# Optimization experiments

Measured on AMD Instinct MI355X. Metric: run time of the kernel, lower is better.

The kernel has to match this reference:

```python
import jax, jax.numpy as jnp
import numpy as np

N_NODES = 100000
N_EDGES = 600000
D = 128
L = 4
BN_EPS = 1e-5


def setup_inputs() -> dict:
    key = jax.random.key(0)
    ks = jax.random.split(key, 12)
    x = jax.random.normal(ks[0], (N_NODES, D), dtype=jnp.float32)
    edge_index = jax.random.randint(ks[1], (2, N_EDGES), 0, N_NODES, dtype=jnp.int64)
    edge_attr = jax.random.uniform(ks[2], (N_EDGES, 1), dtype=jnp.float32)
    s = 0.05
    return {
        'x': x,
        'edge_index': edge_index,
        'edge_attr': edge_attr,
        'We': jax.random.normal(ks[3], (L, 1, D), dtype=jnp.float32) * s,   # GINE edge projection Linear(1, D)
        'be': jnp.zeros((L, D), dtype=jnp.float32),
        'eps': jnp.zeros((L,), dtype=jnp.float32),                          # train_eps=True, init 0
        'W1': jax.random.normal(ks[4], (L, D, D), dtype=jnp.float32) * s,
        'b1': jnp.zeros((L, D), dtype=jnp.float32),
        'gamma': jnp.ones((L, D), dtype=jnp.float32),
        'beta': jnp.zeros((L, D), dtype=jnp.float32),
        'W2': jax.random.normal(ks[5], (L, D, D), dtype=jnp.float32) * s,
        'b2': jnp.zeros((L, D), dtype=jnp.float32),
    }


def _gine_layer(h, src, dst, edge_attr, We, be, eps, W1, b1, gamma, beta, W2, b2):
    n = h.shape[0]
    e = edge_attr @ We + be                       # [E, D] edge embedding
    m = jax.nn.relu(h[src] + e)                   # gather + add + relu (messages)
    agg = jax.ops.segment_sum(m, dst, num_segments=n)  # scatter-add to destination nodes
    z = (1.0 + eps) * h + agg
    # MLP: Linear -> BatchNorm1d (training stats) -> ReLU -> Linear
    z = z @ W1 + b1
    mu = jnp.mean(z, axis=0)
    var = jnp.var(z, axis=0)                      # biased var, as in torch BN training
    z = (z - mu) * jax.lax.rsqrt(var + BN_EPS) * gamma + beta
    z = jax.nn.relu(z)
    return z @ W2 + b2


def reference(x, edge_index, edge_attr, We, be, eps, W1, b1, gamma, beta, W2, b2):
    src, dst = edge_index[0], edge_index[1]
    h = x
    for l in range(L):
        z = _gine_layer(h, src, dst, edge_attr, We[l], be[l], eps[l],
                        W1[l], b1[l], gamma[l], beta[l], W2[l], b2[l])
        r = jax.nn.relu(z)
        h = r if l == 0 else h + r
    return h
```

## Files before the change

kernel.cpp:

```cpp
#include <hip/hip_runtime.h>

#define NN 100000
#define NE 600000
#define DD 128
#define NL 4
#define GB 512

typedef __attribute__((ext_vector_type(8))) short short8;
typedef __attribute__((ext_vector_type(4))) float float4v;
typedef __attribute__((ext_vector_type(2))) float f2;

__device__ inline unsigned short f2bf(float f) {
  union { float f; unsigned u; } v; v.f = f;
  unsigned r = v.u + 0x7fff + ((v.u >> 16) & 1);
  return (unsigned short)(r >> 16);
}
__device__ inline float bf2f(unsigned short u) {
  union { unsigned u; float f; } v; v.u = ((unsigned)u) << 16;
  return v.f;
}
__device__ inline f2 bfpair(unsigned u) {
  f2 r;
  r.x = __uint_as_float(u << 16);
  r.y = __uint_as_float(u & 0xffff0000u);
  return r;
}

__global__ void k_prep(const float* __restrict__ W1, const float* __restrict__ W2,
                       unsigned short* __restrict__ WT, int* __restrict__ counts,
                       float* __restrict__ stats4) {
  int i = blockIdx.x * 256 + threadIdx.x;
  if (i < NN) counts[i] = 0;
  if (i < NL * 256) stats4[i] = 0.f;
  if (i >= 8 * 16384) return;
  int m = i >> 14;
  int el = i & 16383;
  int k = el >> 7;
  int n = el & 127;
  const float* src = (m < 4) ? (W1 + (size_t)m * 16384) : (W2 + (size_t)(m - 4) * 16384);
  WT[(size_t)m * 16384 + n * 128 + k] = f2bf(src[k * 128 + n]);
}

__global__ void k_h2b(const float* __restrict__ src, unsigned short* __restrict__ dst,
                      const int* __restrict__ ei, int* __restrict__ counts) {
  int i = blockIdx.x * 256 + threadIdx.x;
  if (i < NE) atomicAdd(&counts[ei[NE + i]], 1);
  if (i >= NN * DD / 4) return;
  float4 v = ((const float4*)src)[i];
  ushort4 o;
  o.x = f2bf(v.x); o.y = f2bf(v.y); o.z = f2bf(v.z); o.w = f2bf(v.w);
  ((ushort4*)dst)[i] = o;
}

#define ST 256
#define SC 2
#define SB ((NN + ST * SC - 1) / (ST * SC))

__global__ void k_scan_part(const int* __restrict__ counts, int* __restrict__ row_ptr,
                            int* __restrict__ bsums) {
  __shared__ int s[ST];
  int b = blockIdx.x, t = threadIdx.x;
  int base = b * (ST * SC) + t * SC;
  int v0 = (base < NN) ? counts[base] : 0;
  int v1 = (base + 1 < NN) ? counts[base + 1] : 0;
  int tsum = v0 + v1;
  s[t] = tsum;
  __syncthreads();
  for (int d = 1; d < ST; d <<= 1) {
    int x = (t >= d) ? s[t - d] : 0;
    __syncthreads();
    s[t] += x;
    __syncthreads();
  }
  int excl = s[t] - tsum;
  if (base < NN) row_ptr[base] = excl;
  if (base + 1 < NN) row_ptr[base + 1] = excl + v0;
  if (t == ST - 1) bsums[b] = s[t];
}

__global__ void k_scan_bsum(const int* __restrict__ bsums, int* __restrict__ boffs,
                            int* __restrict__ row_ptr) {
  __shared__ int s[ST];
  int t = threadIdx.x;
  int v = (t < SB) ? bsums[t] : 0;
  s[t] = v;
  __syncthreads();
  for (int d = 1; d < ST; d <<= 1) {
    int x = (t >= d) ? s[t - d] : 0;
    __syncthreads();
    s[t] += x;
    __syncthreads();
  }
  if (t < SB) boffs[t] = s[t] - v;
  if (t == ST - 1) row_ptr[NN] = s[t];
}

__global__ void k_scan_add(const int* __restrict__ boffs, int* __restrict__ row_ptr,
                           int* __restrict__ off) {
  int b = blockIdx.x, t = threadIdx.x;
  int base = b * (ST * SC) + t * SC;
  int o = boffs[b];
  if (base < NN) { int v = row_ptr[base] + o; row_ptr[base] = v; off[base] = v; }
  if (base + 1 < NN) { int v = row_ptr[base + 1] + o; row_ptr[base + 1] = v; off[base + 1] = v; }
}

__global__ void k_fill(const int* __restrict__ ei, const float* __restrict__ attr,
                       int* __restrict__ off, int2* __restrict__ csr) {
  int e = blockIdx.x * 256 + threadIdx.x;
  if (e >= NE) return;
  int srcv = ei[e];
  int dstv = ei[NE + e];
  int idx = atomicAdd(&off[dstv], 1);
  csr[idx] = make_int2(srcv, __float_as_int(attr[e]));
}

#define CONS8(hv, at)                                                         \
  do {                                                                        \
    f2 av; av.x = (at); av.y = (at);                                          \
    f2 sx;                                                                    \
    sx = bfpair((hv).x) + (av * we01 + be01);                                 \
    a01 += __builtin_elementwise_max(sx, zero2);                              \
    sx = bfpair((hv).y) + (av * we23 + be23);                                 \
    a23 += __builtin_elementwise_max(sx, zero2);                              \
    sx = bfpair((hv).z) + (av * we45 + be45);                                 \
    a45 += __builtin_elementwise_max(sx, zero2);                              \
    sx = bfpair((hv).w) + (av * we67 + be67);                                 \
    a67 += __builtin_elementwise_max(sx, zero2);                              \
  } while (0)

#define LDROW(s) (*(const uint4*)(hb + (size_t)(s) * DD + d0))

__global__ __launch_bounds__(256) void k_agg(
    const unsigned short* __restrict__ hb,
    const int* __restrict__ row_ptr, const int2* __restrict__ csr,
    const float* __restrict__ We, const float* __restrict__ be,
    const float* __restrict__ epsp, unsigned short* __restrict__ zb) {
  const int tid0 = blockIdx.x * 256 + threadIdx.x;
  const int li = tid0 & 15;
  const int g0 = tid0 >> 4;
  const int NG = (gridDim.x * 256) >> 4;
  const int d0 = li * 8;

  const f2 we01 = *(const f2*)(We + d0);
  const f2 we23 = *(const f2*)(We + d0 + 2);
  const f2 we45 = *(const f2*)(We + d0 + 4);
  const f2 we67 = *(const f2*)(We + d0 + 6);
  const f2 be01 = *(const f2*)(be + d0);
  const f2 be23 = *(const f2*)(be + d0 + 2);
  const f2 be45 = *(const f2*)(be + d0 + 4);
  const f2 be67 = *(const f2*)(be + d0 + 6);
  const float ep = 1.f + epsp[0];
  f2 ep2; ep2.x = ep; ep2.y = ep;
  const f2 zero2 = {0.f, 0.f};

  for (int n = g0; n < NN; n += NG) {
    const int b = row_ptr[n], e = row_ptr[n + 1];
    const int deg = e - b;
    const int cnt = (deg < 16) ? deg : 16;
    int2 rec = (li < cnt) ? csr[b + li] : make_int2(0, 0);
    uint4 hs = LDROW(n);
    const int myidx = rec.x;
    const float myatt = __int_as_float(rec.y);
    f2 a01 = zero2, a23 = zero2, a45 = zero2, a67 = zero2;

    {
      int s0 = __shfl(myidx, 0, 16), s1 = __shfl(myidx, 1, 16);
      int s2 = __shfl(myidx, 2, 16), s3 = __shfl(myidx, 3, 16);
      int s4 = __shfl(myidx, 4, 16), s5 = __shfl(myidx, 5, 16);
      int s6 = __shfl(myidx, 6, 16), s7 = __shfl(myidx, 7, 16);
      float t0 = __shfl(myatt, 0, 16), t1 = __shfl(myatt, 1, 16);
      float t2 = __shfl(myatt, 2, 16), t3 = __shfl(myatt, 3, 16);
      float t4 = __shfl(myatt, 4, 16), t5 = __shfl(myatt, 5, 16);
      float t6 = __shfl(myatt, 6, 16), t7 = __shfl(myatt, 7, 16);
      uint4 h0 = LDROW(s0), h1 = LDROW(s1), h2 = LDROW(s2), h3 = LDROW(s3);
      uint4 h4 = LDROW(s4), h5 = LDROW(s5), h6 = LDROW(s6), h7 = LDROW(s7);
      if (cnt > 0) CONS8(h0, t0);
      if (cnt > 1) CONS8(h1, t1);
      if (cnt > 2) CONS8(h2, t2);
      if (cnt > 3) CONS8(h3, t3);
      if (cnt > 4) CONS8(h4, t4);
      if (cnt > 5) CONS8(h5, t5);
      if (cnt > 6) CONS8(h6, t6);
      if (cnt > 7) CONS8(h7, t7);
    }
    if (deg > 8) {
      int s0 = __shfl(myidx, 8, 16), s1 = __shfl(myidx, 9, 16);
      int s2 = __shfl(myidx, 10, 16), s3 = __shfl(myidx, 11, 16);
      int s4 = __shfl(myidx, 12, 16), s5 = __shfl(myidx, 13, 16);
      int s6 = __shfl(myidx, 14, 16), s7 = __shfl(myidx, 15, 16);
      float t0 = __shfl(myatt, 8, 16), t1 = __shfl(myatt, 9, 16);
      float t2 = __shfl(myatt, 10, 16), t3 = __shfl(myatt, 11, 16);
      float t4 = __shfl(myatt, 12, 16), t5 = __shfl(myatt, 13, 16);
      float t6 = __shfl(myatt, 14, 16), t7 = __shfl(myatt, 15, 16);
      uint4 h0 = LDROW(s0), h1 = LDROW(s1), h2 = LDROW(s2), h3 = LDROW(s3);
      uint4 h4 = LDROW(s4), h5 = LDROW(s5), h6 = LDROW(s6), h7 = LDROW(s7);
      if (cnt > 8)  CONS8(h0, t0);
      if (cnt > 9)  CONS8(h1, t1);
      if (cnt > 10) CONS8(h2, t2);
      if (cnt > 11) CONS8(h3, t3);
      if (cnt > 12) CONS8(h4, t4);
      if (cnt > 13) CONS8(h5, t5);
      if (cnt > 14) CONS8(h6, t6);
      if (cnt > 15) CONS8(h7, t7);
      for (int j = b + 16; j < e; j++) {
        int2 r2 = csr[j];
        float a = __int_as_float(r2.y);
        uint4 hv = LDROW(r2.x);
        CONS8(hv, a);
      }
    }

    f2 z01 = ep2 * bfpair(hs.x) + a01;
    f2 z23 = ep2 * bfpair(hs.y) + a23;
    f2 z45 = ep2 * bfpair(hs.z) + a45;
    f2 z67 = ep2 * bfpair(hs.w) + a67;
    uint4 o;
    o.x = (unsigned)f2bf(z01.x) | ((unsigned)f2bf(z01.y) << 16);
    o.y = (unsigned)f2bf(z23.x) | ((unsigned)f2bf(z23.y) << 16);
    o.z = (unsigned)f2bf(z45.x) | ((unsigned)f2bf(z45.y) << 16);
    o.w = (unsigned)f2bf(z67.x) | ((unsigned)f2bf(z67.y) << 16);
    *(uint4*)(zb + (size_t)n * DD + d0) = o;
  }
}

template <int MODE>
__global__ __launch_bounds__(512) void k_gemm(
    const unsigned short* __restrict__ Xb, const unsigned short* __restrict__ WT,
    const float* __restrict__ bias, float* __restrict__ stats,
    const float* __restrict__ gamma, const float* __restrict__ beta,
    const float* __restrict__ hprev, float* __restrict__ Yout,
    unsigned short* __restrict__ Ybf) {
  __shared__ unsigned short Wl[128 * 136];
  __shared__ unsigned short Xl[2][64 * 136];
  __shared__ float bns[256];
  const int tid = threadIdx.x;
  const int G = gridDim.x;
  const int NT = (NN + 63) >> 6;

  for (int i = tid; i < 2048; i += 512) {
    int rr = i >> 4, c = i & 15;
    *(uint4*)&Wl[rr * 136 + c * 8] = *(const uint4*)&WT[rr * 128 + c * 8];
  }

  const int lane = tid & 63;
  const int w = tid >> 6;
  const int m = lane & 15;
  const int quad = lane >> 4;
  const int rowblk = w & 3;
  const int ctbase = (w >> 2) * 4;

  float4 b4[4];
#pragma unroll
  for (int c = 0; c < 4; c++)
    b4[c] = *(const float4*)&bias[(ctbase + c) * 16 + quad * 4];

  const int c8 = tid & 15, rr16 = tid >> 4;
  float scl[8], sfl[8];
  if (MODE >= 1) {
    if (tid < 128) {
      const float invN = 1.f / (float)NN;
      float mu = stats[tid] * invN;
      float var = fmaxf(stats[128 + tid] * invN - mu * mu, 0.f);
      float xx = var + 1e-5f;
      float r = rsqrtf(xx);
      r = r * (1.5f - 0.5f * xx * r * r);
      float scale = gamma[tid] * r;
      bns[tid] = scale;
      bns[128 + tid] = beta[tid] - mu * scale;
    }
    __syncthreads();
#pragma unroll
    for (int j = 0; j < 8; j++) {
      scl[j] = bns[c8 * 8 + j];
      sfl[j] = bns[128 + c8 * 8 + j];
    }
  }

  uint4 xu[2];
  auto LOADR = [&](int t) {
    int r0 = t << 6;
#pragma unroll
    for (int it = 0; it < 2; it++) {
      int gr = r0 + rr16 + it * 32;
      xu[it] = (gr < NN) ? *(const uint4*)(Xb + (size_t)gr * DD + c8 * 8)
                         : make_uint4(0u, 0u, 0u, 0u);
    }
  };
  auto STORE_LDS = [&](int b) {
#pragma unroll
    for (int it = 0; it < 2; it++) {
      int row = rr16 + it * 32;
      uint4 u = xu[it];
      if (MODE >= 1) {
        unsigned p[4] = {u.x, u.y, u.z, u.w};
#pragma unroll
        for (int j = 0; j < 4; j++) {
          float lo = bf2f((unsigned short)(p[j] & 0xffffu));
          float hi = bf2f((unsigned short)(p[j] >> 16));
          lo = fmaxf(fmaf(lo, scl[2 * j], sfl[2 * j]), 0.f);
          hi = fmaxf(fmaf(hi, scl[2 * j + 1], sfl[2 * j + 1]), 0.f);
          p[j] = (unsigned)f2bf(lo) | ((unsigned)f2bf(hi) << 16);
        }
        u = make_uint4(p[0], p[1], p[2], p[3]);
      }
      *(uint4*)&Xl[b][row * 136 + c8 * 8] = u;
    }
  };

  float4v ssum[4], ssq[4];
  if (MODE == 0) {
#pragma unroll
    for (int c = 0; c < 4; c++) {
      ssum[c] = (float4v){0.f, 0.f, 0.f, 0.f};
      ssq[c] = (float4v){0.f, 0.f, 0.f, 0.f};
    }
  }

  const int t0 = blockIdx.x;
  LOADR(t0);
  STORE_LDS(0);
  if (t0 + G < NT) LOADR(t0 + G);
  __syncthreads();

  int buf = 0;
  for (int t = t0; t < NT; t += G) {
    const int nxt = t + G;
    if (nxt < NT) {
      STORE_LDS(buf ^ 1);
      if (nxt + G < NT) LOADR(nxt + G);
    }

    float4v acc[4];
#pragma unroll
    for (int c = 0; c < 4; c++)
      acc[c] = (float4v){b4[c].x, b4[c].y, b4[c].z, b4[c].w};

    const unsigned short* Ap = &Wl[(ctbase * 16 + m) * 136 + quad * 8];
    const unsigned short* Bp = &Xl[buf][(rowblk * 16 + m) * 136 + quad * 8];
#pragma unroll
    for (int q = 0; q < 4; q++) {
      short8 bfrag = *(const short8*)(Bp + q * 32);
#pragma unroll
      for (int c = 0; c < 4; c++) {
        short8 afrag = *(const short8*)(Ap + c * 16 * 136 + q * 32);
        acc[c] = __builtin_amdgcn_mfma_f32_16x16x32_bf16(afrag, bfrag, acc[c], 0, 0, 0);
      }
    }

    asm volatile("s_waitcnt lgkmcnt(0)" ::: "memory");
    __builtin_amdgcn_s_barrier();

    const int r = (t << 6) + rowblk * 16 + m;
    if (r < NN) {
      const size_t rb = (size_t)r * DD;
#pragma unroll
      for (int c = 0; c < 4; c++) {
        float4v v = acc[c];
        const int col = (ctbase + c) * 16 + quad * 4;
        if (MODE == 0) {
          ssum[c] += v;
          ssq[c] += v * v;
          ushort4 o;
          o.x = f2bf(v[0]); o.y = f2bf(v[1]); o.z = f2bf(v[2]); o.w = f2bf(v[3]);
          *(ushort4*)&Ybf[rb + col] = o;
        } else {
          v[0] = fmaxf(v[0], 0.f); v[1] = fmaxf(v[1], 0.f);
          v[2] = fmaxf(v[2], 0.f); v[3] = fmaxf(v[3], 0.f);
          if (MODE == 2) {
            float4 hp = *(const float4*)&hprev[rb + col];
            v[0] += hp.x; v[1] += hp.y; v[2] += hp.z; v[3] += hp.w;
          }
          *(float4v*)&Yout[rb + col] = v;
          if (Ybf) {
            ushort4 o;
            o.x = f2bf(v[0]); o.y = f2bf(v[1]); o.z = f2bf(v[2]); o.w = f2bf(v[3]);
            *(ushort4*)&Ybf[rb + col] = o;
          }
        }
      }
    }
    buf ^= 1;
  }

  if (MODE == 0) {
    float* sarr = (float*)Xl;
    float* sqarr = sarr + 512;
#pragma unroll
    for (int c = 0; c < 4; c++) {
      float4v s = ssum[c], s2 = ssq[c];
#pragma unroll
      for (int d = 1; d < 16; d <<= 1) {
#pragma unroll
        for (int j = 0; j < 4; j++) {
          s[j] += __shfl_xor(s[j], d);
          s2[j] += __shfl_xor(s2[j], d);
        }
      }
      if (m == 0) {
        *(float4v*)&sarr[w * 64 + c * 16 + quad * 4] = s;
        *(float4v*)&sqarr[w * 64 + c * 16 + quad * 4] = s2;
      }
    }
    __syncthreads();
    if (tid < 128) {
      const int ch = tid >> 6;
      const int cl = tid & 63;
      float s = 0.f, s2 = 0.f;
#pragma unroll
      for (int ww = 0; ww < 4; ww++) {
        s += sarr[(ch * 4 + ww) * 64 + cl];
        s2 += sqarr[(ch * 4 + ww) * 64 + cl];
      }
      atomicAdd(&stats[tid], s);
      atomicAdd(&stats[128 + tid], s2);
    }
  }
}

static inline size_t align256(size_t x) { return (x + 255) & ~(size_t)255; }

extern "C" void kernel_launch(void* const* d_in, const int* in_sizes, int n_in,
                              void* d_out, int out_size, void* d_ws, size_t ws_size,
                              hipStream_t stream) {
  const float* x     = (const float*)d_in[0];
  const int*   ei    = (const int*)d_in[1];
  const float* attr  = (const float*)d_in[2];
  const float* We    = (const float*)d_in[3];
  const float* be    = (const float*)d_in[4];
  const float* eps   = (const float*)d_in[5];
  const float* W1    = (const float*)d_in[6];
  const float* b1    = (const float*)d_in[7];
  const float* gamma = (const float*)d_in[8];
  const float* beta  = (const float*)d_in[9];
  const float* W2    = (const float*)d_in[10];
  const float* b2    = (const float*)d_in[11];
  float* out = (float*)d_out;

  char* w = (char*)d_ws;
  unsigned short* z2 = (unsigned short*)w; w += align256((size_t)NN * DD * 2);
  unsigned short* hb = (unsigned short*)w; w += align256((size_t)NN * DD * 2);
  unsigned short* zb = (unsigned short*)w; w += align256((size_t)NN * DD * 2);
  int*   row_ptr  = (int*)w;   w += align256((size_t)(NN + 1) * 4);
  int*   counts   = (int*)w;   w += align256((size_t)NN * 4);
  int*   off      = (int*)w;   w += align256((size_t)NN * 4);
  int2*  csr      = (int2*)w;  w += align256((size_t)NE * 8);
  float* stats4   = (float*)w; w += align256((size_t)NL * 256 * 4);
  int*   bsums    = (int*)w;   w += align256(ST * 4);
  int*   boffs    = (int*)w;   w += align256(ST * 4);
  unsigned short* WTb = (unsigned short*)w; w += align256((size_t)8 * 16384 * 2);

  k_prep<<<512, 256, 0, stream>>>(W1, W2, WTb, counts, stats4);
  k_h2b<<<(NN * DD / 4 + 255) / 256, 256, 0, stream>>>(x, hb, ei, counts);
  k_scan_part<<<SB, ST, 0, stream>>>(counts, row_ptr, bsums);
  k_scan_bsum<<<1, ST, 0, stream>>>(bsums, boffs, row_ptr);
  k_scan_add<<<SB, ST, 0, stream>>>(boffs, row_ptr, off);
  k_fill<<<(NE + 255) / 256, 256, 0, stream>>>(ei, attr, off, csr);

  for (int l = 0; l < NL; l++) {
    float* st = stats4 + (size_t)l * 256;
    k_agg<<<2048, 256, 0, stream>>>(
        hb, row_ptr, csr, We + l * DD, be + l * DD, eps + l, zb);
    k_gemm<0><<<GB, 512, 0, stream>>>(zb, WTb + (size_t)l * 16384, b1 + l * DD,
                                      st, nullptr, nullptr, nullptr, nullptr, z2);
    unsigned short* hbo = (l < NL - 1) ? hb : nullptr;
    if (l == 0)
      k_gemm<1><<<GB, 512, 0, stream>>>(z2, WTb + (size_t)(4 + l) * 16384, b2 + l * DD,
                                        st, gamma + l * DD, beta + l * DD,
                                        nullptr, out, hbo);
    else
      k_gemm<2><<<GB, 512, 0, stream>>>(z2, WTb + (size_t)(4 + l) * 16384, b2 + l * DD,
                                        st, gamma + l * DD, beta + l * DD,
                                        out, out, hbo);
  }
}
```

Before: 523.9 us.

## Build CSR via two-pass bucketed placement instead of global atomic fill

Replaces the per-edge global atomicAdd CSR fill with a two-phase scheme. Edges are first bucketed by destination block of 512 nodes using shared-memory atomics and coalesced writes to a staging buffer. A per-bucket kernel then places them into the final CSR using shared-memory cursors. This aims to cut scattered global atomics and random writes, at the cost of an extra pass over the edges and an extra NE*8-byte staging buffer.

```diff
diff --git a/kernel.cpp b/kernel.cpp
--- a/kernel.cpp
+++ b/kernel.cpp
@@ -5,6 +5,9 @@
 #define DD 128
 #define NL 4
 #define GB 512
+#define BKS 9
+#define NBK ((NN + 511) >> 9)
+#define CH 4096
 
 typedef __attribute__((ext_vector_type(8))) short short8;
 typedef __attribute__((ext_vector_type(4))) float float4v;
@@ -96,22 +99,83 @@
 }
 
 __global__ void k_scan_add(const int* __restrict__ boffs, int* __restrict__ row_ptr,
-                           int* __restrict__ off) {
+                           int* __restrict__ scur) {
   int b = blockIdx.x, t = threadIdx.x;
   int base = b * (ST * SC) + t * SC;
   int o = boffs[b];
-  if (base < NN) { int v = row_ptr[base] + o; row_ptr[base] = v; off[base] = v; }
-  if (base + 1 < NN) { int v = row_ptr[base + 1] + o; row_ptr[base + 1] = v; off[base + 1] = v; }
-}
-
-__global__ void k_fill(const int* __restrict__ ei, const float* __restrict__ attr,
-                       int* __restrict__ off, int2* __restrict__ csr) {
-  int e = blockIdx.x * 256 + threadIdx.x;
-  if (e >= NE) return;
-  int srcv = ei[e];
-  int dstv = ei[NE + e];
-  int idx = atomicAdd(&off[dstv], 1);
-  csr[idx] = make_int2(srcv, __float_as_int(attr[e]));
+  if (base < NN) {
+    int v = row_ptr[base] + o;
+    row_ptr[base] = v;
+    if ((base & 511) == 0) scur[base >> 9] = v;
+  }
+  if (base + 1 < NN) row_ptr[base + 1] += o;
+}
+
+__global__ __launch_bounds__(256) void k_bucket(
+    const int* __restrict__ ei, const float* __restrict__ attr,
+    int* __restrict__ scur, int2* __restrict__ staging) {
+  __shared__ int cnt[256], cnt2[256], base[256], gbase[256], s[256];
+  __shared__ int lpk[CH];
+  __shared__ int lat[CH];
+  __shared__ unsigned char lbk[CH];
+  const int t = threadIdx.x;
+  const int c0 = blockIdx.x * CH;
+  const int n = min(CH, NE - c0);
+  cnt[t] = 0;
+  cnt2[t] = 0;
+  __syncthreads();
+  for (int k = t; k < n; k += 256) {
+    int dst = ei[NE + c0 + k];
+    atomicAdd(&cnt[dst >> BKS], 1);
+  }
+  __syncthreads();
+  s[t] = cnt[t];
+  __syncthreads();
+  for (int d = 1; d < 256; d <<= 1) {
+    int x = (t >= d) ? s[t - d] : 0;
+    __syncthreads();
+    s[t] += x;
+    __syncthreads();
+  }
+  base[t] = s[t] - cnt[t];
+  if (cnt[t] > 0) gbase[t] = atomicAdd(&scur[t], cnt[t]);
+  __syncthreads();
+  for (int k = t; k < n; k += 256) {
+    int e = c0 + k;
+    int src = ei[e];
+    int dst = ei[NE + e];
+    int b = dst >> BKS;
+    int pos = base[b] + atomicAdd(&cnt2[b], 1);
+    lpk[pos] = src | ((dst & 511) << 17);
+    lat[pos] = __float_as_int(attr[e]);
+    lbk[pos] = (unsigned char)b;
+  }
+  __syncthreads();
+  for (int k = t; k < n; k += 256) {
+    int b = lbk[k];
+    staging[gbase[b] + (k - base[b])] = make_int2(lpk[k], lat[k]);
+  }
+}
+
+__global__ __launch_bounds__(256) void k_place(
+    const int* __restrict__ row_ptr, const int2* __restrict__ staging,
+    int2* __restrict__ csr) {
+  __shared__ int cur[512];
+  const int b = blockIdx.x;
+  const int n0 = b << BKS;
+  const int nb = min(512, NN - n0);
+  const int t = threadIdx.x;
+  for (int j = t; j < nb; j += 256) cur[j] = row_ptr[n0 + j];
+  __syncthreads();
+  const int s0 = row_ptr[n0];
+  const int s1 = row_ptr[n0 + nb];
+  for (int i = s0 + t; i < s1; i += 256) {
+    int2 r = staging[i];
+    int j = ((unsigned)r.x) >> 17;
+    int src = r.x & 0x1FFFF;
+    int slot = atomicAdd(&cur[j], 1);
+    csr[slot] = make_int2(src, r.y);
+  }
 }
 
 #define CONS8(hv, at)                                                         \
@@ -442,8 +506,9 @@
   unsigned short* zb = (unsigned short*)w; w += align256((size_t)NN * DD * 2);
   int*   row_ptr  = (int*)w;   w += align256((size_t)(NN + 1) * 4);
   int*   counts   = (int*)w;   w += align256((size_t)NN * 4);
-  int*   off      = (int*)w;   w += align256((size_t)NN * 4);
+  int*   scur     = (int*)w;   w += align256(256 * 4);
   int2*  csr      = (int2*)w;  w += align256((size_t)NE * 8);
+  int2*  staging  = (int2*)w;  w += align256((size_t)NE * 8);
   float* stats4   = (float*)w; w += align256((size_t)NL * 256 * 4);
   int*   bsums    = (int*)w;   w += align256(ST * 4);
   int*   boffs    = (int*)w;   w += align256(ST * 4);
@@ -453,8 +518,9 @@
   k_h2b<<<(NN * DD / 4 + 255) / 256, 256, 0, stream>>>(x, hb, ei, counts);
   k_scan_part<<<SB, ST, 0, stream>>>(counts, row_ptr, bsums);
   k_scan_bsum<<<1, ST, 0, stream>>>(bsums, boffs, row_ptr);
-  k_scan_add<<<SB, ST, 0, stream>>>(boffs, row_ptr, off);
-  k_fill<<<(NE + 255) / 256, 256, 0, stream>>>(ei, attr, off, csr);
+  k_scan_add<<<SB, ST, 0, stream>>>(boffs, row_ptr, scur);
+  k_bucket<<<(NE + CH - 1) / CH, 256, 0, stream>>>(ei, attr, scur, staging);
+  k_place<<<NBK, 256, 0, stream>>>(row_ptr, staging, csr);
 
   for (int l = 0; l < NL; l++) {
     float* st = stats4 + (size_t)l * 256;
```

Measured after the change: 522.6 us. About the same (-0.2%).
